# Performance work log

Measured on AMD Instinct MI355X. Metric: run time of the kernel, lower is better.

## Reference

```python
import jax, jax.numpy as jnp
import numpy as np

HEADS = 24
KV_HEADS = 6
HEAD_DIM = 64


def _partial_rope(x, cos, sin):
    # x: [B, H, S, head_dim]; cos/sin: [S, rot_dim]; rotate first rot_dim dims
    rot_dim = cos.shape[-1]
    x_rot, x_pass = x[..., :rot_dim], x[..., rot_dim:]
    half = rot_dim // 2
    # use_real_unbind_dim=-2: reshape (..., 2, half) then unbind -> first/second half
    x_real, x_imag = x_rot[..., :half], x_rot[..., half:]
    x_rotated = jnp.concatenate([-x_imag, x_real], axis=-1)
    out = x_rot * cos[None, None] + x_rotated * sin[None, None]
    return jnp.concatenate([out, x_pass], axis=-1)


def setup_inputs() -> dict:
    key = jax.random.key(0)
    ks = jax.random.split(key, 8)
    B, S, D = 2, 2048, 1536
    kv_dim = KV_HEADS * HEAD_DIM
    rot_dim = 32
    hidden_states = jax.random.normal(ks[0], (B, S, D), dtype=jnp.float32)
    # realistic rotary cos/sin from inv-freq angles
    pos = jnp.arange(S, dtype=jnp.float32)
    inv_freq = 1.0 / (10000.0 ** (jnp.arange(0, rot_dim, 2, dtype=jnp.float32) / rot_dim))
    ang = pos[:, None] * inv_freq[None, :]  # [S, rot_dim//2]
    ang = jnp.concatenate([ang, ang], axis=-1)  # [S, rot_dim]
    cos, sin = jnp.cos(ang), jnp.sin(ang)
    Wq = jax.random.normal(ks[1], (D, D), dtype=jnp.float32) * 0.02
    Wk = jax.random.normal(ks[2], (D, kv_dim), dtype=jnp.float32) * 0.02
    Wv = jax.random.normal(ks[3], (D, kv_dim), dtype=jnp.float32) * 0.02
    Wo = jax.random.normal(ks[4], (D, D), dtype=jnp.float32) * 0.02
    bo = jnp.zeros((D,), dtype=jnp.float32)
    return {"hidden_states": hidden_states, "cos": cos, "sin": sin,
            "Wq": Wq, "Wk": Wk, "Wv": Wv, "Wo": Wo, "bo": bo}


def reference(hidden_states, cos, sin, Wq, Wk, Wv, Wo, bo):
    B, S, D = hidden_states.shape
    residual = hidden_states
    q = hidden_states @ Wq  # [B,S,D]
    k = hidden_states @ Wk  # [B,S,kv_dim]
    v = hidden_states @ Wv
    q = q.reshape(B, S, HEADS, HEAD_DIM).transpose(0, 2, 1, 3)       # [B,H,S,d]
    k = k.reshape(B, S, KV_HEADS, HEAD_DIM).transpose(0, 2, 1, 3)    # [B,Hkv,S,d]
    v = v.reshape(B, S, KV_HEADS, HEAD_DIM).transpose(0, 2, 1, 3)
    rep = HEADS // KV_HEADS
    k = jnp.repeat(k, rep, axis=1)  # GQA repeat_interleave -> [B,H,S,d]
    v = jnp.repeat(v, rep, axis=1)
    # partial RoPE on query and key (self-attention)
    q = _partial_rope(q, cos, sin)
    k = _partial_rope(k, cos, sin)
    scale = 1.0 / jnp.sqrt(jnp.float32(HEAD_DIM))
    scores = jnp.einsum('bhqd,bhkd->bhqk', q, k) * scale
    probs = jax.nn.softmax(scores, axis=-1)
    out = jnp.einsum('bhqk,bhkd->bhqd', probs, v)
    out = out.transpose(0, 2, 1, 3).reshape(B, S, D)
    out = out @ Wo + bo
    return out + residual
```

## Files before the change

### kernel.cpp

```cpp
#include <hip/hip_runtime.h>

#define HEADS 24
#define KVH   6
#define HD    64
#define BB    2
#define SS    2048
#define DD    1536
#define KVD   384
#define QKD   1920
#define MM    4096

typedef unsigned short ushort_t;
typedef __attribute__((ext_vector_type(8))) short short8;
typedef __attribute__((ext_vector_type(4))) short short4v;
typedef __attribute__((ext_vector_type(4))) float f32x4;

__device__ __forceinline__ ushort_t f2bf(float f) {
    union { float f; unsigned u; } v; v.f = f;
    return (ushort_t)((v.u + 0x8000u) >> 16);
}
__device__ __forceinline__ unsigned pk2(float a, float b) {
    union { float f; unsigned u; } x, y; x.f = a; y.f = b;
    return ((x.u + 0x8000u) >> 16) | (((y.u + 0x8000u) >> 16) << 16);
}
__device__ __forceinline__ unsigned pk2t(float a, float b) {
    union { float f; unsigned u; } x, y; x.f = a; y.f = b;
    return (x.u >> 16) | (y.u & 0xFFFF0000u);
}
__device__ __forceinline__ float fexp2(float s) {
    float t = fmaf(s, 8388608.0f, 1065055420.0f);
    union { int i; float f; } v; v.i = (int)t;
    return v.f;
}
__device__ __forceinline__ short8 lds_frag8(const ushort_t* p) {
    short4v lo = *(const short4v*)p;
    short4v hi = *(const short4v*)(p + 4);
    return __builtin_shufflevector(lo, hi, 0, 1, 2, 3, 4, 5, 6, 7);
}
__device__ __forceinline__ void glds16(const void* g, void* l) {
    __builtin_amdgcn_global_load_lds(
        (const __attribute__((address_space(1))) void*)g,
        (__attribute__((address_space(3))) void*)l, 16, 0, 0);
}

__device__ __forceinline__ void tconv_body(const float* __restrict__ in,
                                           ushort_t* __restrict__ out,
                                           int R, int C, int cb, int rb)
{
    __shared__ ushort_t tile[32][33];
    const int tx = threadIdx.x & 31, ty = threadIdx.x >> 5;
    const int c0 = cb * 32, r0 = rb * 32;
#pragma unroll
    for (int i = 0; i < 4; ++i)
        tile[ty + i * 8][tx] = f2bf(in[(size_t)(r0 + ty + i * 8) * C + c0 + tx]);
    __syncthreads();
#pragma unroll
    for (int i = 0; i < 4; ++i)
        out[(size_t)(c0 + ty + i * 8) * R + r0 + tx] = tile[tx][ty + i * 8];
}

#define NCVT (MM * DD / 4 / 256)
__global__ __launch_bounds__(256) void k_prep(const float* __restrict__ HS,
                                              const float* __restrict__ Wq,
                                              const float* __restrict__ Wk,
                                              const float* __restrict__ Wv,
                                              const float* __restrict__ Wo,
                                              ushort_t* __restrict__ Xbf,
                                              ushort_t* __restrict__ Wqt,
                                              ushort_t* __restrict__ Wkt,
                                              ushort_t* __restrict__ Wvt,
                                              ushort_t* __restrict__ Wot)
{
    int bid = blockIdx.x;
    if (bid < NCVT) {
        int i = bid * 256 + threadIdx.x;
        float4 v = ((const float4*)HS)[i];
        uint2 o = { pk2(v.x, v.y), pk2(v.z, v.w) };
        ((uint2*)Xbf)[i] = o;
        return;
    }
    bid -= NCVT;
    if (bid < 2304) { tconv_body(Wq, Wqt, DD, DD,  bid % 48, bid / 48); return; }
    bid -= 2304;
    if (bid < 576)  { tconv_body(Wk, Wkt, DD, KVD, bid % 12, bid / 12); return; }
    bid -= 576;
    if (bid < 576)  { tconv_body(Wv, Wvt, DD, KVD, bid % 12, bid / 12); return; }
    bid -= 576;
    tconv_body(Wo, Wot, DD, DD, bid % 48, bid / 48);
}

__global__ __launch_bounds__(256) void k_proj(const ushort_t* __restrict__ Xbf,
                                              const ushort_t* __restrict__ Wqt,
                                              const ushort_t* __restrict__ Wkt,
                                              const ushort_t* __restrict__ Wvt,
                                              const float* __restrict__ cosb,
                                              const float* __restrict__ sinb,
                                              ushort_t* __restrict__ QKVb,
                                              ushort_t* __restrict__ VT)
{
    __shared__ ushort_t As[128][32];
    __shared__ ushort_t Bs[128][32];
    const int t = threadIdx.x, lane = t & 63, wave = t >> 6;
    const int n16 = lane & 15, quad = lane >> 4;
    const int wr = wave >> 1, wc = wave & 1;
    const int srow = lane >> 2;
    const int scol = (lane & 3) * 8;

    if (blockIdx.x < 480) {
        const int nt = blockIdx.x % 15;
        const int n0 = nt * 128;
        const int m0 = (blockIdx.x / 15) * 128;
        const ushort_t* Bt; int nl, isq;
        if (nt < 12) { Bt = Wqt; nl = n0;      isq = 1; }
        else         { Bt = Wkt; nl = n0 - DD; isq = 0; }

        const size_t aoff0 = (size_t)(m0 + wave * 16 + srow) * DD + scol;
        const size_t aoff1 = (size_t)(m0 + (wave + 4) * 16 + srow) * DD + scol;
        const size_t boff0 = (size_t)(nl + wave * 16 + srow) * DD + scol;
        const size_t boff1 = (size_t)(nl + (wave + 4) * 16 + srow) * DD + scol;
        ushort_t* lA0 = &As[wave * 16][0];
        ushort_t* lA1 = &As[(wave + 4) * 16][0];
        ushort_t* lB0 = &Bs[wave * 16][0];
        ushort_t* lB1 = &Bs[(wave + 4) * 16][0];

        f32x4 acc[4][4] = {};
        for (int k0 = 0; k0 < DD; k0 += 32) {
            __syncthreads();
            glds16(Xbf + aoff0 + k0, lA0);
            glds16(Xbf + aoff1 + k0, lA1);
            glds16(Bt  + boff0 + k0, lB0);
            glds16(Bt  + boff1 + k0, lB1);
            __syncthreads();
            short8 af[4], bf8[4];
#pragma unroll
            for (int i = 0; i < 4; ++i) af[i]  = *(const short8*)&As[wr * 64 + i * 16 + n16][quad * 8];
#pragma unroll
            for (int j = 0; j < 4; ++j) bf8[j] = *(const short8*)&Bs[wc * 64 + j * 16 + n16][quad * 8];
#pragma unroll
            for (int i = 0; i < 4; ++i)
#pragma unroll
                for (int j = 0; j < 4; ++j)
                    acc[i][j] = __builtin_amdgcn_mfma_f32_16x16x32_bf16(af[i], bf8[j], acc[i][j], 0, 0, 0);
        }

        const float QSC = 0.18033688011112042f;
#pragma unroll
        for (int i = 0; i < 4; ++i) {
#pragma unroll
            for (int r = 0; r < 4; ++r) {
                const int row = m0 + wr * 64 + i * 16 + quad * 4 + r;
                ushort_t* outp = QKVb + (size_t)row * QKD + n0 + wc * 64 + n16;
                float v0 = acc[i][0][r], v1 = acc[i][1][r];
                float v2 = acc[i][2][r], v3 = acc[i][3][r];
                {
                    const int s = row & (SS - 1);
                    float c0 = cosb[s * 32 + n16],      s0 = sinb[s * 32 + n16];
                    float c1 = cosb[s * 32 + 16 + n16], s1 = sinb[s * 32 + 16 + n16];
                    float nr = v0 * c0 - v1 * s0;
                    float ni = v1 * c1 + v0 * s1;
                    v0 = nr; v1 = ni;
                }
                if (isq) { v0 *= QSC; v1 *= QSC; v2 *= QSC; v3 *= QSC; }
                outp[0]  = f2bf(v0);
                outp[16] = f2bf(v1);
                outp[32] = f2bf(v2);
                outp[48] = f2bf(v3);
            }
        }
    } else {
        const int vb = blockIdx.x - 480;
        const int n0 = (vb & 31) * 128;
        const int m0 = (vb >> 5) * 64;

        const size_t aoff  = (size_t)(m0 + wave * 16 + srow) * DD + scol;
        const size_t boff0 = (size_t)(n0 + wave * 32 + srow) * DD + scol;
        const size_t boff1 = boff0 + (size_t)16 * DD;
        ushort_t* lA  = &As[wave * 16][0];
        ushort_t* lB0 = &Bs[wave * 32][0];
        ushort_t* lB1 = &Bs[wave * 32 + 16][0];

        f32x4 acc[2][4] = {};
        for (int k0 = 0; k0 < DD; k0 += 32) {
            __syncthreads();
            glds16(Wvt + aoff  + k0, lA);
            glds16(Xbf + boff0 + k0, lB0);
            glds16(Xbf + boff1 + k0, lB1);
            __syncthreads();
            short8 af[2], bf8[4];
#pragma unroll
            for (int i = 0; i < 2; ++i) af[i]  = *(const short8*)&As[wr * 32 + i * 16 + n16][quad * 8];
#pragma unroll
            for (int j = 0; j < 4; ++j) bf8[j] = *(const short8*)&Bs[wc * 64 + j * 16 + n16][quad * 8];
#pragma unroll
            for (int i = 0; i < 2; ++i)
#pragma unroll
                for (int j = 0; j < 4; ++j)
                    acc[i][j] = __builtin_amdgcn_mfma_f32_16x16x32_bf16(af[i], bf8[j], acc[i][j], 0, 0, 0);
        }

        const int b = n0 >> 11;
        const int s0 = 8 * (n16 >> 2) + 2 * (n16 & 3);
#pragma unroll
        for (int i = 0; i < 2; ++i)
#pragma unroll
            for (int r = 0; r < 4; ++r) {
                const int c = m0 + wr * 32 + i * 16 + quad * 4 + r;
                ushort_t* op = VT + ((size_t)b * KVD + c) * SS +
                               (n0 & (SS - 1)) + wc * 64 + s0;
                *(unsigned*)op        = pk2(acc[i][0][r], acc[i][1][r]);
                *(unsigned*)(op + 32) = pk2(acc[i][2][r], acc[i][3][r]);
            }
    }
}

__global__ __launch_bounds__(512, 6) void k_attn(const ushort_t* __restrict__ QKVb,
                                                 const ushort_t* __restrict__ VT,
                                                 ushort_t* __restrict__ AOb)
{
    __shared__ __align__(16) ushort_t Ks[2][64][76];
    __shared__ __align__(16) ushort_t Vs[2][64][76];

    const int t    = threadIdx.x;
    const int wave = t >> 6;
    const int quad = (t >> 4) & 3;
    const int n16  = t & 15;
    const int q0   = blockIdx.x * 128;
    const int h    = blockIdx.y;
    const int b    = blockIdx.z;
    const int kh   = h >> 2;

    const int sr = t >> 3;
    const int sc = (t & 7) * 8;

    short8 qf[2];
#pragma unroll
    for (int kc = 0; kc < 2; ++kc)
        qf[kc] = *(const short8*)(QKVb +
            (size_t)(b * SS + q0 + wave * 16 + n16) * QKD +
            h * HD + kc * 32 + quad * 8);

    float l_p = 0.0f;
    f32x4 acc_o[4] = {};

    const ushort_t* Kbase = QKVb + (size_t)(b * SS) * QKD + DD + kh * HD;
    const ushort_t* Vbase = VT + ((size_t)b * KVD + kh * 64) * SS;

    uint4 kv, vv;

#define LOAD_TILE(K0) do {                                                  \
        kv = *(const uint4*)(Kbase + (size_t)((K0) + sr) * QKD + sc);       \
        vv = *(const uint4*)(Vbase + (size_t)sr * SS + (K0) + sc);          \
    } while (0)

#define WRITE_BUF(BI) do {                                                  \
        *(uint2*)&Ks[BI][sr][sc]     = make_uint2(kv.x, kv.y);              \
        *(uint2*)&Ks[BI][sr][sc + 4] = make_uint2(kv.z, kv.w);              \
        *(uint2*)&Vs[BI][sr][sc]     = make_uint2(vv.x, vv.y);              \
        *(uint2*)&Vs[BI][sr][sc + 4] = make_uint2(vv.z, vv.w);              \
    } while (0)

    LOAD_TILE(0);
    WRITE_BUF(0);
    LOAD_TILE(64);
    __syncthreads();

    const int NT = SS / 64;
    for (int kt = 0; kt < NT; ++kt) {
        const int cur = kt & 1;
        const ushort_t (*Kc)[76] = Ks[cur];
        const ushort_t (*Vc)[76] = Vs[cur];

        f32x4 sT[4] = {};
#pragma unroll
        for (int kc = 0; kc < 2; ++kc) {
            short8 bf[4];
#pragma unroll
            for (int jj = 0; jj < 4; ++jj)
                bf[jj] = lds_frag8(&Kc[jj * 16 + n16][kc * 32 + quad * 8]);
#pragma unroll
            for (int jj = 0; jj < 4; ++jj)
                sT[jj] = __builtin_amdgcn_mfma_f32_16x16x32_bf16(
                    bf[jj], qf[kc], sT[jj], 0, 0, 0);
        }

        union PB { unsigned w[4]; short8 v; };
        PB pb[2];
#pragma unroll
        for (int w = 0; w < 4; ++w) {
            float p0 = fexp2(sT[0][w]);
            float p1 = fexp2(sT[1][w]);
            float p2 = fexp2(sT[2][w]);
            float p3 = fexp2(sT[3][w]);
            pb[0].w[w] = pk2t(p0, p1);
            pb[1].w[w] = pk2t(p2, p3);
            l_p += (p0 + p1) + (p2 + p3);
        }

#pragma unroll
        for (int kc = 0; kc < 2; ++kc) {
            short8 vb[4];
#pragma unroll
            for (int dd = 0; dd < 4; ++dd)
                vb[dd] = lds_frag8(&Vc[dd * 16 + n16][kc * 32 + quad * 8]);
#pragma unroll
            for (int dd = 0; dd < 4; ++dd)
                acc_o[dd] = __builtin_amdgcn_mfma_f32_16x16x32_bf16(
                    vb[dd], pb[kc].v, acc_o[dd], 0, 0, 0);
        }

        if (kt + 1 < NT) {
            WRITE_BUF(cur ^ 1);
            if (kt + 2 < NT)
                LOAD_TILE((kt + 2) * 64);
            __syncthreads();
        }
    }
#undef LOAD_TILE
#undef WRITE_BUF

    {
        float s = l_p;
        s += __shfl_xor(s, 16);
        s += __shfl_xor(s, 32);
        const float inv = 1.0f / s;
        const int q = q0 + wave * 16 + n16;
        ushort_t* op = AOb + (size_t)(b * SS + q) * DD + h * HD + quad * 4;
#pragma unroll
        for (int dd = 0; dd < 4; ++dd) {
            uint2 o = { pk2(acc_o[dd][0] * inv, acc_o[dd][1] * inv),
                        pk2(acc_o[dd][2] * inv, acc_o[dd][3] * inv) };
            *(uint2*)(op + dd * 16) = o;
        }
    }
}

__global__ __launch_bounds__(256) void k_out_mfma(const ushort_t* __restrict__ AOb,
                                                  const ushort_t* __restrict__ Wot,
                                                  const float* __restrict__ bo,
                                                  const float* __restrict__ HS,
                                                  float* __restrict__ out)
{
    __shared__ ushort_t As[64][32];
    __shared__ ushort_t Bs[128][32];
    const int t = threadIdx.x, lane = t & 63, wave = t >> 6;
    const int n16 = lane & 15, quad = lane >> 4;
    const int wr = wave >> 1, wc = wave & 1;
    const int n0 = blockIdx.x * 128;
    const int m0 = blockIdx.y * 64;

    const int srow = lane >> 2;
    const int scol = (lane & 3) * 8;
    const size_t aoff  = (size_t)(m0 + wave * 16 + srow) * DD + scol;
    const size_t boff0 = (size_t)(n0 + wave * 32 + srow) * DD + scol;
    const size_t boff1 = boff0 + (size_t)16 * DD;
    ushort_t* lA  = &As[wave * 16][0];
    ushort_t* lB0 = &Bs[wave * 32][0];
    ushort_t* lB1 = &Bs[wave * 32 + 16][0];

    f32x4 acc[2][4] = {};
    for (int k0 = 0; k0 < DD; k0 += 32) {
        __syncthreads();
        glds16(AOb + aoff  + k0, lA);
        glds16(Wot + boff0 + k0, lB0);
        glds16(Wot + boff1 + k0, lB1);
        __syncthreads();
        short8 af[2], bf8[4];
#pragma unroll
        for (int i = 0; i < 2; ++i) af[i]  = *(const short8*)&As[wr * 32 + i * 16 + n16][quad * 8];
#pragma unroll
        for (int j = 0; j < 4; ++j) bf8[j] = *(const short8*)&Bs[wc * 64 + j * 16 + n16][quad * 8];
#pragma unroll
        for (int i = 0; i < 2; ++i)
#pragma unroll
            for (int j = 0; j < 4; ++j)
                acc[i][j] = __builtin_amdgcn_mfma_f32_16x16x32_bf16(af[i], bf8[j], acc[i][j], 0, 0, 0);
    }

    const int colb = n0 + wc * 64 + n16;
    float bo4[4];
#pragma unroll
    for (int j = 0; j < 4; ++j) bo4[j] = bo[colb + j * 16];
#pragma unroll
    for (int i = 0; i < 2; ++i) {
#pragma unroll
        for (int r = 0; r < 4; ++r) {
            const int row = m0 + wr * 32 + i * 16 + quad * 4 + r;
            float* op = out + (size_t)row * DD + colb;
            const float* hp = HS + (size_t)row * DD + colb;
#pragma unroll
            for (int j = 0; j < 4; ++j)
                op[j * 16] = acc[i][j][r] + bo4[j] + hp[j * 16];
        }
    }
}

extern "C" void kernel_launch(void* const* d_in, const int* in_sizes, int n_in,
                              void* d_out, int out_size, void* d_ws, size_t ws_size,
                              hipStream_t stream)
{
    const float* HS   = (const float*)d_in[0];
    const float* cosb = (const float*)d_in[1];
    const float* sinb = (const float*)d_in[2];
    const float* Wq   = (const float*)d_in[3];
    const float* Wk   = (const float*)d_in[4];
    const float* Wv   = (const float*)d_in[5];
    const float* Wo   = (const float*)d_in[6];
    const float* bo   = (const float*)d_in[7];
    float* out = (float*)d_out;

    ushort_t* Xbf  = (ushort_t*)d_ws;
    ushort_t* QKVb = Xbf  + (size_t)MM * DD;
    ushort_t* AOb  = QKVb + (size_t)MM * QKD;
    ushort_t* Wqt  = AOb  + (size_t)MM * DD;
    ushort_t* Wkt  = Wqt  + (size_t)DD * DD;
    ushort_t* Wvt  = Wkt  + (size_t)KVD * DD;
    ushort_t* Wot  = Wvt  + (size_t)KVD * DD;
    ushort_t* VT   = Wot  + (size_t)DD * DD;

    const int nprep = NCVT + 2304 + 576 + 576 + 2304;
    k_prep    <<<dim3(nprep), 256, 0, stream>>>(HS, Wq, Wk, Wv, Wo,
                                                Xbf, Wqt, Wkt, Wvt, Wot);
    k_proj    <<<dim3(480 + 192), 256, 0, stream>>>(Xbf, Wqt, Wkt, Wvt,
                                                    cosb, sinb, QKVb, VT);
    k_attn    <<<dim3(SS / 128, HEADS, BB), 512, 0, stream>>>(QKVb, VT, AOb);
    k_out_mfma<<<dim3(DD / 128, MM / 64),   256, 0, stream>>>(AOb, Wot, bo, HS, out);
}
```

Before: 248.1 us.

## Double GEMM K-tile to 64 with XOR-swizzled LDS layout in projection and output

```diff
diff --git a/kernel.cpp b/kernel.cpp
--- a/kernel.cpp
+++ b/kernel.cpp
@@ -98,13 +98,14 @@
                                               ushort_t* __restrict__ QKVb,
                                               ushort_t* __restrict__ VT)
 {
-    __shared__ ushort_t As[128][32];
-    __shared__ ushort_t Bs[128][32];
+    __shared__ ushort_t As[128][64];
+    __shared__ ushort_t Bs[128][64];
     const int t = threadIdx.x, lane = t & 63, wave = t >> 6;
     const int n16 = lane & 15, quad = lane >> 4;
     const int wr = wave >> 1, wc = wave & 1;
-    const int srow = lane >> 2;
-    const int scol = (lane & 3) * 8;
+    const int sr8 = lane >> 3;
+    const int swc = ((lane & 7) ^ sr8) * 8;
+    const int cx  = n16 & 7;
 
     if (blockIdx.x < 480) {
         const int nt = blockIdx.x % 15;
@@ -114,33 +115,31 @@
         if (nt < 12) { Bt = Wqt; nl = n0;      isq = 1; }
         else         { Bt = Wkt; nl = n0 - DD; isq = 0; }
 
-        const size_t aoff0 = (size_t)(m0 + wave * 16 + srow) * DD + scol;
-        const size_t aoff1 = (size_t)(m0 + (wave + 4) * 16 + srow) * DD + scol;
-        const size_t boff0 = (size_t)(nl + wave * 16 + srow) * DD + scol;
-        const size_t boff1 = (size_t)(nl + (wave + 4) * 16 + srow) * DD + scol;
-        ushort_t* lA0 = &As[wave * 16][0];
-        ushort_t* lA1 = &As[(wave + 4) * 16][0];
-        ushort_t* lB0 = &Bs[wave * 16][0];
-        ushort_t* lB1 = &Bs[(wave + 4) * 16][0];
-
         f32x4 acc[4][4] = {};
-        for (int k0 = 0; k0 < DD; k0 += 32) {
+        for (int k0 = 0; k0 < DD; k0 += 64) {
             __syncthreads();
-            glds16(Xbf + aoff0 + k0, lA0);
-            glds16(Xbf + aoff1 + k0, lA1);
-            glds16(Bt  + boff0 + k0, lB0);
-            glds16(Bt  + boff1 + k0, lB1);
+#pragma unroll
+            for (int o = 0; o < 128; o += 32) {
+                glds16(Xbf + (size_t)(m0 + o + wave * 8 + sr8) * DD + k0 + swc,
+                       &As[o + wave * 8][0]);
+                glds16(Bt  + (size_t)(nl + o + wave * 8 + sr8) * DD + k0 + swc,
+                       &Bs[o + wave * 8][0]);
+            }
             __syncthreads();
-            short8 af[4], bf8[4];
-#pragma unroll
-            for (int i = 0; i < 4; ++i) af[i]  = *(const short8*)&As[wr * 64 + i * 16 + n16][quad * 8];
-#pragma unroll
-            for (int j = 0; j < 4; ++j) bf8[j] = *(const short8*)&Bs[wc * 64 + j * 16 + n16][quad * 8];
-#pragma unroll
-            for (int i = 0; i < 4; ++i)
-#pragma unroll
-                for (int j = 0; j < 4; ++j)
-                    acc[i][j] = __builtin_amdgcn_mfma_f32_16x16x32_bf16(af[i], bf8[j], acc[i][j], 0, 0, 0);
+#pragma unroll
+            for (int kc2 = 0; kc2 < 2; ++kc2) {
+                const int ch = (((kc2 << 2) | quad) ^ cx) * 8;
+                short8 af[4], bf8[4];
+#pragma unroll
+                for (int i = 0; i < 4; ++i) af[i]  = *(const short8*)&As[wr * 64 + i * 16 + n16][ch];
+#pragma unroll
+                for (int j = 0; j < 4; ++j) bf8[j] = *(const short8*)&Bs[wc * 64 + j * 16 + n16][ch];
+#pragma unroll
+                for (int i = 0; i < 4; ++i)
+#pragma unroll
+                    for (int j = 0; j < 4; ++j)
+                        acc[i][j] = __builtin_amdgcn_mfma_f32_16x16x32_bf16(af[i], bf8[j], acc[i][j], 0, 0, 0);
+            }
         }
 
         const float QSC = 0.18033688011112042f;
@@ -172,30 +171,32 @@
         const int n0 = (vb & 31) * 128;
         const int m0 = (vb >> 5) * 64;
 
-        const size_t aoff  = (size_t)(m0 + wave * 16 + srow) * DD + scol;
-        const size_t boff0 = (size_t)(n0 + wave * 32 + srow) * DD + scol;
-        const size_t boff1 = boff0 + (size_t)16 * DD;
-        ushort_t* lA  = &As[wave * 16][0];
-        ushort_t* lB0 = &Bs[wave * 32][0];
-        ushort_t* lB1 = &Bs[wave * 32 + 16][0];
-
         f32x4 acc[2][4] = {};
-        for (int k0 = 0; k0 < DD; k0 += 32) {
+        for (int k0 = 0; k0 < DD; k0 += 64) {
             __syncthreads();
-            glds16(Wvt + aoff  + k0, lA);
-            glds16(Xbf + boff0 + k0, lB0);
-            glds16(Xbf + boff1 + k0, lB1);
+#pragma unroll
+            for (int o = 0; o < 64; o += 32)
+                glds16(Wvt + (size_t)(m0 + o + wave * 8 + sr8) * DD + k0 + swc,
+                       &As[o + wave * 8][0]);
+#pragma unroll
+            for (int o = 0; o < 128; o += 32)
+                glds16(Xbf + (size_t)(n0 + o + wave * 8 + sr8) * DD + k0 + swc,
+                       &Bs[o + wave * 8][0]);
             __syncthreads();
-            short8 af[2], bf8[4];
-#pragma unroll
-            for (int i = 0; i < 2; ++i) af[i]  = *(const short8*)&As[wr * 32 + i * 16 + n16][quad * 8];
-#pragma unroll
-            for (int j = 0; j < 4; ++j) bf8[j] = *(const short8*)&Bs[wc * 64 + j * 16 + n16][quad * 8];
-#pragma unroll
-            for (int i = 0; i < 2; ++i)
-#pragma unroll
-                for (int j = 0; j < 4; ++j)
-                    acc[i][j] = __builtin_amdgcn_mfma_f32_16x16x32_bf16(af[i], bf8[j], acc[i][j], 0, 0, 0);
+#pragma unroll
+            for (int kc2 = 0; kc2 < 2; ++kc2) {
+                const int ch = (((kc2 << 2) | quad) ^ cx) * 8;
+                short8 af[2], bf8[4];
+#pragma unroll
+                for (int i = 0; i < 2; ++i) af[i]  = *(const short8*)&As[wr * 32 + i * 16 + n16][ch];
+#pragma unroll
+                for (int j = 0; j < 4; ++j) bf8[j] = *(const short8*)&Bs[wc * 64 + j * 16 + n16][ch];
+#pragma unroll
+                for (int i = 0; i < 2; ++i)
+#pragma unroll
+                    for (int j = 0; j < 4; ++j)
+                        acc[i][j] = __builtin_amdgcn_mfma_f32_16x16x32_bf16(af[i], bf8[j], acc[i][j], 0, 0, 0);
+            }
         }
 
         const int b = n0 >> 11;
@@ -340,40 +341,44 @@
                                                   const float* __restrict__ HS,
                                                   float* __restrict__ out)
 {
-    __shared__ ushort_t As[64][32];
-    __shared__ ushort_t Bs[128][32];
+    __shared__ ushort_t As[64][64];
+    __shared__ ushort_t Bs[128][64];
     const int t = threadIdx.x, lane = t & 63, wave = t >> 6;
     const int n16 = lane & 15, quad = lane >> 4;
     const int wr = wave >> 1, wc = wave & 1;
     const int n0 = blockIdx.x * 128;
     const int m0 = blockIdx.y * 64;
 
-    const int srow = lane >> 2;
-    const int scol = (lane & 3) * 8;
-    const size_t aoff  = (size_t)(m0 + wave * 16 + srow) * DD + scol;
-    const size_t boff0 = (size_t)(n0 + wave * 32 + srow) * DD + scol;
-    const size_t boff1 = boff0 + (size_t)16 * DD;
-    ushort_t* lA  = &As[wave * 16][0];
-    ushort_t* lB0 = &Bs[wave * 32][0];
-    ushort_t* lB1 = &Bs[wave * 32 + 16][0];
+    const int sr8 = lane >> 3;
+    const int swc = ((lane & 7) ^ sr8) * 8;
+    const int cx  = n16 & 7;
 
     f32x4 acc[2][4] = {};
-    for (int k0 = 0; k0 < DD; k0 += 32) {
+    for (int k0 = 0; k0 < DD; k0 += 64) {
         __syncthreads();
-        glds16(AOb + aoff  + k0, lA);
-        glds16(Wot + boff0 + k0, lB0);
-        glds16(Wot + boff1 + k0, lB1);
+#pragma unroll
+        for (int o = 0; o < 64; o += 32)
+            glds16(AOb + (size_t)(m0 + o + wave * 8 + sr8) * DD + k0 + swc,
+                   &As[o + wave * 8][0]);
+#pragma unroll
+        for (int o = 0; o < 128; o += 32)
+            glds16(Wot + (size_t)(n0 + o + wave * 8 + sr8) * DD + k0 + swc,
+                   &Bs[o + wave * 8][0]);
         __syncthreads();
-        short8 af[2], bf8[4];
-#pragma unroll
-        for (int i = 0; i < 2; ++i) af[i]  = *(const short8*)&As[wr * 32 + i * 16 + n16][quad * 8];
-#pragma unroll
-        for (int j = 0; j < 4; ++j) bf8[j] = *(const short8*)&Bs[wc * 64 + j * 16 + n16][quad * 8];
-#pragma unroll
-        for (int i = 0; i < 2; ++i)
-#pragma unroll
-            for (int j = 0; j < 4; ++j)
-                acc[i][j] = __builtin_amdgcn_mfma_f32_16x16x32_bf16(af[i], bf8[j], acc[i][j], 0, 0, 0);
+#pragma unroll
+        for (int kc2 = 0; kc2 < 2; ++kc2) {
+            const int ch = (((kc2 << 2) | quad) ^ cx) * 8;
+            short8 af[2], bf8[4];
+#pragma unroll
+            for (int i = 0; i < 2; ++i) af[i]  = *(const short8*)&As[wr * 32 + i * 16 + n16][ch];
+#pragma unroll
+            for (int j = 0; j < 4; ++j) bf8[j] = *(const short8*)&Bs[wc * 64 + j * 16 + n16][ch];
+#pragma unroll
+            for (int i = 0; i < 2; ++i)
+#pragma unroll
+                for (int j = 0; j < 4; ++j)
+                    acc[i][j] = __builtin_amdgcn_mfma_f32_16x16x32_bf16(af[i], bf8[j], acc[i][j], 0, 0, 0);
+        }
     }
 
     const int colb = n0 + wc * 64 + n16;
```

Result: no change. 250.1 us (+0.8%).
